# Optimization experiments

Measured on AMD Instinct MI355X. Metric: run time of the kernel, lower is better.

## Reference

```python
import jax, jax.numpy as jnp
import numpy as np

B, T, E, H, L, V, CTX = 16, 1024, 512, 8, 6, 32, 1024
HD = E // H


def setup_inputs() -> dict:
    key = jax.random.key(0)
    ks = jax.random.split(key, 20)
    s = 0.02
    inp = {
        "tokens": jax.random.randint(ks[0], (B, T), 0, V),
        "emb": jax.random.normal(ks[1], (V, E), jnp.float32) * s,
        "pos_emb": jax.random.normal(ks[2], (CTX, E), jnp.float32) * s,
        "Wq": jax.random.normal(ks[3], (L, H, E, HD), jnp.float32) * s,
        "Wk": jax.random.normal(ks[4], (L, H, E, HD), jnp.float32) * s,
        "Wv": jax.random.normal(ks[5], (L, H, E, HD), jnp.float32) * s,
        "Wo": jax.random.normal(ks[6], (L, E, E), jnp.float32) * s,
        "bo": jnp.zeros((L, E), jnp.float32),
        "ln1_g": jnp.ones((L, E), jnp.float32),
        "ln1_b": jnp.zeros((L, E), jnp.float32),
        "ln2_g": jnp.ones((L, E), jnp.float32),
        "ln2_b": jnp.zeros((L, E), jnp.float32),
        "W1": jax.random.normal(ks[7], (L, E, E), jnp.float32) * s,
        "b1": jnp.zeros((L, E), jnp.float32),
        "W2": jax.random.normal(ks[8], (L, E, E), jnp.float32) * s,
        "b2": jnp.zeros((L, E), jnp.float32),
        "lnf_g": jnp.ones((E,), jnp.float32),
        "lnf_b": jnp.zeros((E,), jnp.float32),
        "Wf": jax.random.normal(ks[9], (E, V), jnp.float32) * s,
        "bf": jnp.zeros((V,), jnp.float32),
    }
    return inp


def _layernorm(x, g, b, eps=1e-5):
    mu = x.mean(-1, keepdims=True)
    var = ((x - mu) ** 2).mean(-1, keepdims=True)
    return (x - mu) * jax.lax.rsqrt(var + eps) * g + b


def reference(tokens, emb, pos_emb, Wq, Wk, Wv, Wo, bo, ln1_g, ln1_b,
              ln2_g, ln2_b, W1, b1, W2, b2, lnf_g, lnf_b, Wf, bf):
    Bt, Tt = tokens.shape
    x = emb[tokens] + pos_emb[:Tt]  # [B,T,E]
    causal = jnp.tril(jnp.ones((Tt, Tt), bool))

    def block(x, p):
        wq, wk, wv, wo, bo_, g1, b1_, g2, b2_, w1, bb1, w2, bb2 = p
        h = _layernorm(x, g1, b1_)
        q = jnp.einsum('bte,hed->bhtd', h, wq)
        k = jnp.einsum('bte,hed->bhtd', h, wk)
        v = jnp.einsum('bte,hed->bhtd', h, wv)
        # NOTE: source applies NO 1/sqrt(d) scaling
        s = jnp.einsum('bhtd,bhsd->bhts', q, k)
        s = jnp.where(causal, s, -jnp.inf)
        a = jax.nn.softmax(s, axis=-1)
        o = jnp.einsum('bhts,bhsd->bhtd', a, v)
        o = o.transpose(0, 2, 1, 3).reshape(Bt, Tt, E)  # concat heads
        x = x + jnp.einsum('bte,ef->btf', o, wo) + bo_
        h2 = _layernorm(x, g2, b2_)
        f = jax.nn.relu(jnp.einsum('bte,ef->btf', h2, w1) + bb1)
        f = jnp.einsum('bte,ef->btf', f, w2) + bb2
        return x + f, None

    x, _ = jax.lax.scan(block, x, (Wq, Wk, Wv, Wo, bo, ln1_g, ln1_b,
                                   ln2_g, ln2_b, W1, b1, W2, b2))
    x = _layernorm(x, lnf_g, lnf_b)
    logits = jnp.einsum('bte,ev->btv', x, Wf) + bf
    return logits
```

## Files before the change

kernel.cpp:

```cpp
#include <hip/hip_runtime.h>
#include <hip/hip_bf16.h>

namespace {

constexpr int B = 16, T = 1024, E = 512, H = 8, L = 6, V = 32, HD = 64;
constexpr int BT = B * T;
constexpr long S = (long)BT * E;
constexpr int QS = 1536;

typedef __attribute__((ext_vector_type(8))) short bf16x8;
typedef __attribute__((ext_vector_type(4))) float f32x4;

__device__ inline float b2f(ushort u) {
  union { unsigned u; float f; } v; v.u = (unsigned)u << 16; return v.f;
}
__device__ inline ushort f2b(float f) {
  union { float f; unsigned u; } v; v.f = f;
  unsigned r = v.u + 0x7FFFu + ((v.u >> 16) & 1u);
  return (ushort)(r >> 16);
}
__device__ inline void gl_lds16(const ushort* g, ushort* lds) {
  __builtin_amdgcn_global_load_lds(
      (const __attribute__((address_space(1))) void*)g,
      (__attribute__((address_space(3))) void*)lds, 16, 0, 0);
}

__global__ void embed_kernel(const int* __restrict__ tokens,
                             const float* __restrict__ emb,
                             const float* __restrict__ pos,
                             float* __restrict__ x) {
  int idx = blockIdx.x * blockDim.x + threadIdx.x;
  constexpr int TOT = BT * (E / 4);
  if (idx >= TOT) return;
  int row = idx >> 7, c4 = idx & 127;
  int t = row & (T - 1);
  int tok = tokens[row];
  float4 a = reinterpret_cast<const float4*>(emb + (long)tok * E)[c4];
  float4 p = reinterpret_cast<const float4*>(pos + (long)t * E)[c4];
  float4 r;
  r.x = a.x + p.x; r.y = a.y + p.y; r.z = a.z + p.z; r.w = a.w + p.w;
  reinterpret_cast<float4*>(x + (long)row * E)[c4] = r;
}

__global__ __launch_bounds__(256)
void wconv_kernel(const float* __restrict__ in, ushort* __restrict__ out,
                  int K, int Nn, int ppl, long layer_stride, long off) {
  const int z = blockIdx.z;
  const long pin = (long)z * K * Nn;
  const long pout = (long)(z / ppl) * layer_stride + off +
                    (long)(z % ppl) * Nn * K;
  __shared__ float t[32][33];
  const int k0 = blockIdx.x * 32, n0 = blockIdx.y * 32;
  const int tid = threadIdx.x, r = tid >> 5, c = tid & 31;
  #pragma unroll
  for (int i = 0; i < 4; i++)
    t[r + i * 8][c] = in[pin + (long)(k0 + r + i * 8) * Nn + n0 + c];
  __syncthreads();
  #pragma unroll
  for (int i = 0; i < 4; i++)
    out[pout + (long)(n0 + r + i * 8) * K + k0 + c] = f2b(t[c][r + i * 8]);
}

__global__ __launch_bounds__(128)
void ln_kernel(const float* __restrict__ x, const float* __restrict__ g,
               const float* __restrict__ b, ushort* __restrict__ out) {
  int row = blockIdx.x, tid = threadIdx.x;
  float4 v = reinterpret_cast<const float4*>(x + (long)row * E)[tid];
  float s = v.x + v.y + v.z + v.w;
  #pragma unroll
  for (int off = 32; off > 0; off >>= 1) s += __shfl_down(s, off, 64);
  __shared__ float r1[2], r2[2];
  int lane = tid & 63, wid = tid >> 6;
  if (lane == 0) r1[wid] = s;
  __syncthreads();
  float mean = (r1[0] + r1[1]) * (1.0f / E);
  float4 d;
  d.x = v.x - mean; d.y = v.y - mean; d.z = v.z - mean; d.w = v.w - mean;
  float s2 = d.x * d.x + d.y * d.y + d.z * d.z + d.w * d.w;
  #pragma unroll
  for (int off = 32; off > 0; off >>= 1) s2 += __shfl_down(s2, off, 64);
  if (lane == 0) r2[wid] = s2;
  __syncthreads();
  float rstd = rsqrtf((r2[0] + r2[1]) * (1.0f / E) + 1e-5f);
  float4 gg = reinterpret_cast<const float4*>(g)[tid];
  float4 bb = reinterpret_cast<const float4*>(b)[tid];
  ushort4 o;
  o.x = f2b(d.x * rstd * gg.x + bb.x);
  o.y = f2b(d.y * rstd * gg.y + bb.y);
  o.z = f2b(d.z * rstd * gg.z + bb.z);
  o.w = f2b(d.w * rstd * gg.w + bb.w);
  reinterpret_cast<ushort4*>(out + (long)row * E)[tid] = o;
}

template <int MODE>
__global__ __launch_bounds__(256, 3)
void bgemm_kernel(const ushort* __restrict__ A, const ushort* __restrict__ Bt,
                  const float* __restrict__ bias, const float* __restrict__ res,
                  void* __restrict__ Cout, int Nl) {
  constexpr int K = 512;
  __shared__ ushort As[128][32];
  __shared__ ushort Bs[128][32];
  const int tid = threadIdx.x, lane = tid & 63, wid = tid >> 6;
  const int bm = blockIdx.x * 128, bn = blockIdx.y * 128;
  const int wm = (wid >> 1) * 64, wn = (wid & 1) * 64;
  const int lo = lane & 15, hi = lane >> 4;
  const int arow = lane >> 2, acol = (lane & 3) * 8;
  f32x4 acc[4][4] = {};
  for (int k0 = 0; k0 < K; k0 += 32) {
    #pragma unroll
    for (int i = 0; i < 2; i++) {
      int seg = wid * 2 + i;
      gl_lds16(A + (long)(bm + seg * 16 + arow) * K + k0 + acol,
               &As[seg * 16][0]);
      gl_lds16(Bt + (long)(bn + seg * 16 + arow) * K + k0 + acol,
               &Bs[seg * 16][0]);
    }
    __syncthreads();
    bf16x8 af[4], bfr[4];
    #pragma unroll
    for (int mi = 0; mi < 4; mi++)
      af[mi] = *(const bf16x8*)&As[wm + mi * 16 + lo][hi * 8];
    #pragma unroll
    for (int ni = 0; ni < 4; ni++)
      bfr[ni] = *(const bf16x8*)&Bs[wn + ni * 16 + lo][hi * 8];
    #pragma unroll
    for (int mi = 0; mi < 4; mi++)
      #pragma unroll
      for (int ni = 0; ni < 4; ni++)
        acc[mi][ni] = __builtin_amdgcn_mfma_f32_16x16x32_bf16(
            af[mi], bfr[ni], acc[mi][ni], 0, 0, 0);
    __syncthreads();
  }
  #pragma unroll
  for (int mi = 0; mi < 4; mi++) {
    #pragma unroll
    for (int ni = 0; ni < 4; ni++) {
      const int gn = bn + wn + ni * 16 + lo;
      const float bv = (MODE >= 1) ? bias[gn] : 0.f;
      #pragma unroll
      for (int r = 0; r < 4; r++) {
        const long gm = bm + wm + mi * 16 + hi * 4 + r;
        float vv = acc[mi][ni][r];
        if (MODE == 0) {
          ((ushort*)Cout)[gm * Nl + gn] = f2b(vv);
        } else if (MODE == 1) {
          ((float*)Cout)[gm * Nl + gn] = vv + bv + res[gm * Nl + gn];
        } else {
          ((ushort*)Cout)[gm * Nl + gn] = f2b(fmaxf(vv + bv, 0.f));
        }
      }
    }
  }
}

__global__ __launch_bounds__(256, 2)
void attn_kernel(const ushort* __restrict__ qkv, ushort* __restrict__ o) {
  const int b = blockIdx.z, h = blockIdx.y;
  const int qt = (gridDim.x - 1) - blockIdx.x;
  const int tid = threadIdx.x, wid = tid >> 6, lane = tid & 63;
  const int lo = lane & 15, hi = lane >> 4;
  const long bh = (long)b * T;
  const int qbase = qt * 128 + wid * 32;
  const int dch = qt * 2 + (wid >> 1);
  const int roff = 32 * (wid & 1);
  constexpr float SHIFT = 12.0f;
  __shared__ ushort Ks[64 * 64];
  __shared__ ushort Vs[64 * 64];
  __shared__ ushort Ps[4][32 * 64];
  char* KsB = (char*)Ks;
  char* VsB = (char*)Vs;
  char* PsB = (char*)Ps[wid];

  bf16x8 qf[2][2];
  #pragma unroll
  for (int mf = 0; mf < 2; mf++)
    #pragma unroll
    for (int kh = 0; kh < 2; kh++)
      qf[mf][kh] = *(const bf16x8*)(qkv + (bh + qbase + mf * 16 + lo) * QS +
                                    h * 64 + kh * 32 + hi * 8);
  f32x4 accO[2][4] = {};
  float lsum[2][4];
  #pragma unroll
  for (int a = 0; a < 2; a++)
    #pragma unroll
    for (int r = 0; r < 4; r++) lsum[a][r] = 0.f;

  const ushort* kb = qkv + bh * QS + 512 + h * 64;
  const ushort* vb = qkv + bh * QS + 1024 + h * 64;
  const int nch = qt * 2 + 2;

  for (int c = 0; c < nch; c++) {
    const long s0 = (long)c * 64;
    #pragma unroll
    for (int it = 0; it < 2; it++) {
      int idx = it * 256 + tid;
      int key = idx >> 3, c8 = idx & 7;
      uint4 kv = *(const uint4*)(kb + (s0 + key) * QS + c8 * 8);
      *(uint4*)(KsB + ((key * 128 + c8 * 16) ^ ((key & 7) << 4))) = kv;
    }
    {
      const int key0 = (tid & 31) * 2, dim0 = (tid >> 5) * 8;
      uint4 v0 = *(const uint4*)(vb + (s0 + key0) * QS + dim0);
      uint4 v1 = *(const uint4*)(vb + (s0 + key0 + 1) * QS + dim0);
      const ushort* p0 = (const ushort*)&v0;
      const ushort* p1 = (const ushort*)&v1;
      #pragma unroll
      for (int j = 0; j < 8; j++) {
        const int dim = dim0 + j;
        ushort2 w; w.x = p0[j]; w.y = p1[j];
        *(ushort2*)(VsB + ((dim * 128 + key0 * 2) ^ ((dim & 7) << 4))) = w;
      }
    }
    __syncthreads();
    if (c <= dch) {
      const bool diag = (c == dch);
      bf16x8 kf[4][2];
      #pragma unroll
      for (int nf = 0; nf < 4; nf++)
        #pragma unroll
        for (int kh = 0; kh < 2; kh++) {
          const int key = nf * 16 + lo;
          kf[nf][kh] = *(const bf16x8*)(
              KsB + ((key * 128 + kh * 64 + hi * 16) ^ ((key & 7) << 4)));
        }
      #pragma unroll
      for (int mf = 0; mf < 2; mf++) {
        f32x4 s[4];
        #pragma unroll
        for (int nf = 0; nf < 4; nf++) {
          f32x4 z = {0.f, 0.f, 0.f, 0.f};
          z = __builtin_amdgcn_mfma_f32_16x16x32_bf16(qf[mf][0], kf[nf][0],
                                                      z, 0, 0, 0);
          z = __builtin_amdgcn_mfma_f32_16x16x32_bf16(qf[mf][1], kf[nf][1],
                                                      z, 0, 0, 0);
          s[nf] = z;
        }
        if (diag) {
          #pragma unroll
          for (int nf = 0; nf < 4; nf++)
            #pragma unroll
            for (int r = 0; r < 4; r++)
              if (nf * 16 + lo > roff + mf * 16 + hi * 4 + r)
                s[nf][r] = -1e30f;
        }
        #pragma unroll
        for (int r = 0; r < 4; r++) {
          float p0 = __expf(s[0][r] - SHIFT), p1 = __expf(s[1][r] - SHIFT);
          float p2 = __expf(s[2][r] - SHIFT), p3 = __expf(s[3][r] - SHIFT);
          lsum[mf][r] += (p0 + p1) + (p2 + p3);
          const int ql = mf * 16 + hi * 4 + r;
          const int swz = (ql & 7) << 4;
          *(ushort*)(PsB + ((ql * 128 + (lo) * 2) ^ swz))      = f2b(p0);
          *(ushort*)(PsB + ((ql * 128 + (16 + lo) * 2) ^ swz)) = f2b(p1);
          *(ushort*)(PsB + ((ql * 128 + (32 + lo) * 2) ^ swz)) = f2b(p2);
          *(ushort*)(PsB + ((ql * 128 + (48 + lo) * 2) ^ swz)) = f2b(p3);
        }
      }
      asm volatile("s_waitcnt lgkmcnt(0)" ::: "memory");
      #pragma unroll
      for (int ks = 0; ks < 2; ks++) {
        bf16x8 pa[2];
        #pragma unroll
        for (int mf = 0; mf < 2; mf++) {
          const int ql = mf * 16 + lo;
          pa[mf] = *(const bf16x8*)(
              PsB + ((ql * 128 + ks * 64 + hi * 16) ^ ((ql & 7) << 4)));
        }
        #pragma unroll
        for (int nd = 0; nd < 4; nd++) {
          const int dim = nd * 16 + lo;
          bf16x8 vf = *(const bf16x8*)(
              VsB + ((dim * 128 + ks * 64 + hi * 16) ^ ((dim & 7) << 4)));
          #pragma unroll
          for (int mf = 0; mf < 2; mf++)
            accO[mf][nd] = __builtin_amdgcn_mfma_f32_16x16x32_bf16(
                pa[mf], vf, accO[mf][nd], 0, 0, 0);
        }
      }
    }
    __syncthreads();
  }
  #pragma unroll
  for (int mf = 0; mf < 2; mf++)
    #pragma unroll
    for (int r = 0; r < 4; r++) {
      float l = lsum[mf][r];
      #pragma unroll
      for (int msk = 1; msk < 16; msk <<= 1) l += __shfl_xor(l, msk, 64);
      lsum[mf][r] = 1.0f / l;
    }
  #pragma unroll
  for (int mf = 0; mf < 2; mf++)
    #pragma unroll
    for (int nd = 0; nd < 4; nd++)
      #pragma unroll
      for (int r = 0; r < 4; r++) {
        const int ql = mf * 16 + hi * 4 + r, dim = nd * 16 + lo;
        *(ushort*)(PsB + ql * 128 + dim * 2) =
            f2b(accO[mf][nd][r] * lsum[mf][r]);
      }
  asm volatile("s_waitcnt lgkmcnt(0)" ::: "memory");
  #pragma unroll
  for (int it = 0; it < 4; it++) {
    const int idx = it * 64 + lane;
    const int row = idx >> 3, c8 = idx & 7;
    uint4 val = *(const uint4*)(PsB + row * 128 + c8 * 16);
    *(uint4*)(o + (bh + qbase + row) * E + h * 64 + c8 * 8) = val;
  }
}

__global__ __launch_bounds__(256)
void logits_kernel(const ushort* __restrict__ xf, const ushort* __restrict__ WfT,
                   const float* __restrict__ bf, float* __restrict__ out) {
  __shared__ float xs[8][E];
  const int row0 = blockIdx.x * 8, tid = threadIdx.x;
  #pragma unroll
  for (int i = 0; i < 4; i++) {
    int idx = i * 256 + tid;
    int r = idx >> 7, c4 = idx & 127;
    ushort4 u = ((const ushort4*)(xf + (long)(row0 + r) * E))[c4];
    float4 f;
    f.x = b2f(u.x); f.y = b2f(u.y); f.z = b2f(u.z); f.w = b2f(u.w);
    *(float4*)&xs[r][c4 * 4] = f;
  }
  __syncthreads();
  const int r = tid >> 5, c = tid & 31;
  float acc = 0.f;
  for (int e8 = 0; e8 < 64; e8++) {
    uint4 w = *(const uint4*)(WfT + (long)c * E + e8 * 8);
    const ushort* ws = (const ushort*)&w;
    #pragma unroll
    for (int j = 0; j < 8; j++) acc += xs[r][e8 * 8 + j] * b2f(ws[j]);
  }
  out[(long)(row0 + r) * V + c] = acc + bf[c];
}

}

extern "C" void kernel_launch(void* const* d_in, const int* in_sizes, int n_in,
                              void* d_out, int out_size, void* d_ws,
                              size_t ws_size, hipStream_t stream) {
  const int*   tokens = (const int*)d_in[0];
  const float* emb    = (const float*)d_in[1];
  const float* pos    = (const float*)d_in[2];
  const float* Wq     = (const float*)d_in[3];
  const float* Wk     = (const float*)d_in[4];
  const float* Wv     = (const float*)d_in[5];
  const float* Wo     = (const float*)d_in[6];
  const float* bo     = (const float*)d_in[7];
  const float* ln1g   = (const float*)d_in[8];
  const float* ln1b   = (const float*)d_in[9];
  const float* ln2g   = (const float*)d_in[10];
  const float* ln2b   = (const float*)d_in[11];
  const float* W1     = (const float*)d_in[12];
  const float* b1     = (const float*)d_in[13];
  const float* W2     = (const float*)d_in[14];
  const float* b2     = (const float*)d_in[15];
  const float* lnfg   = (const float*)d_in[16];
  const float* lnfb   = (const float*)d_in[17];
  const float* Wf     = (const float*)d_in[18];
  const float* bf     = (const float*)d_in[19];
  float* out = (float*)d_out;

  char* p = (char*)d_ws;
  float*  x    = (float*)p;          p += S * 4;
  ushort* hb   = (ushort*)p;         p += S * 2;
  ushort* qkvb = (ushort*)p;         p += (long)BT * QS * 2;
  const long WSZ = (long)L * E * E;
  ushort* wqkvT = (ushort*)p;        p += (long)L * QS * E * 2;
  ushort* woT  = (ushort*)p;         p += WSZ * 2;
  ushort* w1T  = (ushort*)p;         p += WSZ * 2;
  ushort* w2T  = (ushort*)p;         p += WSZ * 2;
  ushort* wfT  = (ushort*)p;         p += (long)E * V * 2;

  const long QLS = (long)QS * E;

  wconv_kernel<<<dim3(16, 2, L * H), 256, 0, stream>>>(Wq, wqkvT, E, HD, H,
                                                       QLS, 0);
  wconv_kernel<<<dim3(16, 2, L * H), 256, 0, stream>>>(Wk, wqkvT, E, HD, H,
                                                       QLS, (long)512 * E);
  wconv_kernel<<<dim3(16, 2, L * H), 256, 0, stream>>>(Wv, wqkvT, E, HD, H,
                                                       QLS, (long)1024 * E);
  wconv_kernel<<<dim3(16, 16, L), 256, 0, stream>>>(Wo, woT, E, E, 1,
                                                    (long)E * E, 0);
  wconv_kernel<<<dim3(16, 16, L), 256, 0, stream>>>(W1, w1T, E, E, 1,
                                                    (long)E * E, 0);
  wconv_kernel<<<dim3(16, 16, L), 256, 0, stream>>>(W2, w2T, E, E, 1,
                                                    (long)E * E, 0);
  wconv_kernel<<<dim3(16, 1, 1), 256, 0, stream>>>(Wf, wfT, E, V, 1,
                                                   (long)E * V, 0);

  embed_kernel<<<(BT * (E / 4) + 255) / 256, 256, 0, stream>>>(tokens, emb,
                                                               pos, x);

  const dim3 gq(BT / 128, QS / 128);
  const dim3 gg(BT / 128, E / 128);
  const dim3 ga(T / 128, H, B);

  for (int l = 0; l < L; l++) {
    const long wo = (long)l * E * E;
    ln_kernel<<<BT, 128, 0, stream>>>(x, ln1g + l * E, ln1b + l * E, hb);
    bgemm_kernel<0><<<gq, 256, 0, stream>>>(hb, wqkvT + l * QLS, nullptr,
                                            nullptr, qkvb, QS);
    attn_kernel<<<ga, 256, 0, stream>>>(qkvb, hb);
    bgemm_kernel<1><<<gg, 256, 0, stream>>>(hb, woT + wo, bo + l * E, x, x,
                                            E);
    ln_kernel<<<BT, 128, 0, stream>>>(x, ln2g + l * E, ln2b + l * E, hb);
    bgemm_kernel<2><<<gg, 256, 0, stream>>>(hb, w1T + wo, b1 + l * E, nullptr,
                                            qkvb, E);
    bgemm_kernel<1><<<gg, 256, 0, stream>>>((ushort*)qkvb, w2T + wo,
                                            b2 + l * E, x, x, E);
  }

  ln_kernel<<<BT, 128, 0, stream>>>(x, lnfg, lnfb, hb);
  logits_kernel<<<BT / 8, 256, 0, stream>>>(hb, wfT, bf, out);
}
```

Before: 1.348 ms.

## Double GEMM K-tile to 64 and use 128-key attention chunks with diagonal trimming

The GEMM now stages a 64-wide K slice per iteration, halving the number of barrier-separated loop trips and issuing twice as many MFMAs between syncs. The attention kernel processes 128-key chunks instead of 64, so there are half as many K/V load and barrier rounds. On the diagonal chunk each wave limits its QK and PV loops to the keys it actually needs instead of idling. This costs more LDS per block (larger K, V and P tiles), which may lower occupancy, and the attention inner loops become runtime-bounded rather than fully unrolled.

After: 1.451 ms. 1.08x slower.

```diff
diff --git a/kernel.cpp b/kernel.cpp
--- a/kernel.cpp
+++ b/kernel.cpp
@@ -98,37 +98,43 @@
                   const float* __restrict__ bias, const float* __restrict__ res,
                   void* __restrict__ Cout, int Nl) {
   constexpr int K = 512;
-  __shared__ ushort As[128][32];
-  __shared__ ushort Bs[128][32];
+  __shared__ ushort As[128][64];
+  __shared__ ushort Bs[128][64];
   const int tid = threadIdx.x, lane = tid & 63, wid = tid >> 6;
   const int bm = blockIdx.x * 128, bn = blockIdx.y * 128;
   const int wm = (wid >> 1) * 64, wn = (wid & 1) * 64;
   const int lo = lane & 15, hi = lane >> 4;
-  const int arow = lane >> 2, acol = (lane & 3) * 8;
+  const int arow = lane >> 3, acol = (lane & 7) * 8;
   f32x4 acc[4][4] = {};
-  for (int k0 = 0; k0 < K; k0 += 32) {
-    #pragma unroll
-    for (int i = 0; i < 2; i++) {
-      int seg = wid * 2 + i;
-      gl_lds16(A + (long)(bm + seg * 16 + arow) * K + k0 + acol,
-               &As[seg * 16][0]);
-      gl_lds16(Bt + (long)(bn + seg * 16 + arow) * K + k0 + acol,
-               &Bs[seg * 16][0]);
+  for (int k0 = 0; k0 < K; k0 += 64) {
+    #pragma unroll
+    for (int i = 0; i < 4; i++) {
+      int seg = wid * 4 + i;
+      gl_lds16(A + (long)(bm + seg * 8 + arow) * K + k0 + acol,
+               &As[seg * 8][0]);
+      gl_lds16(Bt + (long)(bn + seg * 8 + arow) * K + k0 + acol,
+               &Bs[seg * 8][0]);
     }
     __syncthreads();
-    bf16x8 af[4], bfr[4];
+    bf16x8 af[4][2], bfr[4][2];
     #pragma unroll
     for (int mi = 0; mi < 4; mi++)
-      af[mi] = *(const bf16x8*)&As[wm + mi * 16 + lo][hi * 8];
+      #pragma unroll
+      for (int kh = 0; kh < 2; kh++)
+        af[mi][kh] = *(const bf16x8*)&As[wm + mi * 16 + lo][kh * 32 + hi * 8];
     #pragma unroll
     for (int ni = 0; ni < 4; ni++)
-      bfr[ni] = *(const bf16x8*)&Bs[wn + ni * 16 + lo][hi * 8];
-    #pragma unroll
-    for (int mi = 0; mi < 4; mi++)
-      #pragma unroll
-      for (int ni = 0; ni < 4; ni++)
-        acc[mi][ni] = __builtin_amdgcn_mfma_f32_16x16x32_bf16(
-            af[mi], bfr[ni], acc[mi][ni], 0, 0, 0);
+      #pragma unroll
+      for (int kh = 0; kh < 2; kh++)
+        bfr[ni][kh] = *(const bf16x8*)&Bs[wn + ni * 16 + lo][kh * 32 + hi * 8];
+    #pragma unroll
+    for (int kh = 0; kh < 2; kh++)
+      #pragma unroll
+      for (int mi = 0; mi < 4; mi++)
+        #pragma unroll
+        for (int ni = 0; ni < 4; ni++)
+          acc[mi][ni] = __builtin_amdgcn_mfma_f32_16x16x32_bf16(
+              af[mi][kh], bfr[ni][kh], acc[mi][ni], 0, 0, 0);
     __syncthreads();
   }
   #pragma unroll
@@ -161,12 +167,11 @@
   const int lo = lane & 15, hi = lane >> 4;
   const long bh = (long)b * T;
   const int qbase = qt * 128 + wid * 32;
-  const int dch = qt * 2 + (wid >> 1);
-  const int roff = 32 * (wid & 1);
+  const int roff = wid * 32;
   constexpr float SHIFT = 12.0f;
-  __shared__ ushort Ks[64 * 64];
-  __shared__ ushort Vs[64 * 64];
-  __shared__ ushort Ps[4][32 * 64];
+  __shared__ ushort Ks[128 * 64];
+  __shared__ ushort Vs[64 * 128];
+  __shared__ ushort Ps[4][32 * 128];
   char* KsB = (char*)Ks;
   char* VsB = (char*)Vs;
   char* PsB = (char*)Ps[wid];
@@ -187,90 +192,87 @@
 
   const ushort* kb = qkv + bh * QS + 512 + h * 64;
   const ushort* vb = qkv + bh * QS + 1024 + h * 64;
-  const int nch = qt * 2 + 2;
+  const int nch = qt + 1;
 
   for (int c = 0; c < nch; c++) {
-    const long s0 = (long)c * 64;
-    #pragma unroll
-    for (int it = 0; it < 2; it++) {
+    const long s0 = (long)c * 128;
+    #pragma unroll
+    for (int it = 0; it < 4; it++) {
       int idx = it * 256 + tid;
       int key = idx >> 3, c8 = idx & 7;
       uint4 kv = *(const uint4*)(kb + (s0 + key) * QS + c8 * 8);
       *(uint4*)(KsB + ((key * 128 + c8 * 16) ^ ((key & 7) << 4))) = kv;
     }
     {
-      const int key0 = (tid & 31) * 2, dim0 = (tid >> 5) * 8;
-      uint4 v0 = *(const uint4*)(vb + (s0 + key0) * QS + dim0);
-      uint4 v1 = *(const uint4*)(vb + (s0 + key0 + 1) * QS + dim0);
-      const ushort* p0 = (const ushort*)&v0;
-      const ushort* p1 = (const ushort*)&v1;
+      const int key0 = (tid & 63) * 2, dim0 = (tid >> 6) * 16;
+      uint4 va0 = *(const uint4*)(vb + (s0 + key0) * QS + dim0);
+      uint4 va1 = *(const uint4*)(vb + (s0 + key0) * QS + dim0 + 8);
+      uint4 vb0 = *(const uint4*)(vb + (s0 + key0 + 1) * QS + dim0);
+      uint4 vb1 = *(const uint4*)(vb + (s0 + key0 + 1) * QS + dim0 + 8);
+      const ushort* pa_ = (const ushort*)&va0;
+      const ushort* pa2 = (const ushort*)&va1;
+      const ushort* pb_ = (const ushort*)&vb0;
+      const ushort* pb2 = (const ushort*)&vb1;
       #pragma unroll
       for (int j = 0; j < 8; j++) {
         const int dim = dim0 + j;
-        ushort2 w; w.x = p0[j]; w.y = p1[j];
-        *(ushort2*)(VsB + ((dim * 128 + key0 * 2) ^ ((dim & 7) << 4))) = w;
+        ushort2 w; w.x = pa_[j]; w.y = pb_[j];
+        *(ushort2*)(VsB + ((dim * 256 + key0 * 2) ^ ((dim & 7) << 4))) = w;
+      }
+      #pragma unroll
+      for (int j = 0; j < 8; j++) {
+        const int dim = dim0 + 8 + j;
+        ushort2 w; w.x = pa2[j]; w.y = pb2[j];
+        *(ushort2*)(VsB + ((dim * 256 + key0 * 2) ^ ((dim & 7) << 4))) = w;
       }
     }
     __syncthreads();
-    if (c <= dch) {
-      const bool diag = (c == dch);
-      bf16x8 kf[4][2];
-      #pragma unroll
-      for (int nf = 0; nf < 4; nf++)
+    {
+      const bool diag = (c == qt);
+      const int nfLim = diag ? (roff / 16 + 2) : 8;
+      const int ksLim = diag ? (roff / 32 + 1) : 4;
+      for (int nf = 0; nf < nfLim; nf++) {
+        const int key = nf * 16 + lo;
+        const int kswz = (key & 7) << 4;
+        bf16x8 kf0 = *(const bf16x8*)(KsB + ((key * 128 + hi * 16) ^ kswz));
+        bf16x8 kf1 =
+            *(const bf16x8*)(KsB + ((key * 128 + 64 + hi * 16) ^ kswz));
         #pragma unroll
-        for (int kh = 0; kh < 2; kh++) {
-          const int key = nf * 16 + lo;
-          kf[nf][kh] = *(const bf16x8*)(
-              KsB + ((key * 128 + kh * 64 + hi * 16) ^ ((key & 7) << 4)));
-        }
-      #pragma unroll
-      for (int mf = 0; mf < 2; mf++) {
-        f32x4 s[4];
-        #pragma unroll
-        for (int nf = 0; nf < 4; nf++) {
+        for (int mf = 0; mf < 2; mf++) {
           f32x4 z = {0.f, 0.f, 0.f, 0.f};
-          z = __builtin_amdgcn_mfma_f32_16x16x32_bf16(qf[mf][0], kf[nf][0],
-                                                      z, 0, 0, 0);
-          z = __builtin_amdgcn_mfma_f32_16x16x32_bf16(qf[mf][1], kf[nf][1],
-                                                      z, 0, 0, 0);
-          s[nf] = z;
-        }
-        if (diag) {
-          #pragma unroll
-          for (int nf = 0; nf < 4; nf++)
+          z = __builtin_amdgcn_mfma_f32_16x16x32_bf16(qf[mf][0], kf0, z,
+                                                      0, 0, 0);
+          z = __builtin_amdgcn_mfma_f32_16x16x32_bf16(qf[mf][1], kf1, z,
+                                                      0, 0, 0);
+          if (diag) {
             #pragma unroll
             for (int r = 0; r < 4; r++)
-              if (nf * 16 + lo > roff + mf * 16 + hi * 4 + r)
-                s[nf][r] = -1e30f;
+              if (key > roff + mf * 16 + hi * 4 + r) z[r] = -1e30f;
+          }
+          #pragma unroll
+          for (int r = 0; r < 4; r++) {
+            float p = __expf(z[r] - SHIFT);
+            lsum[mf][r] += p;
+            const int ql = mf * 16 + hi * 4 + r;
+            *(ushort*)(PsB + ((ql * 256 + key * 2) ^ ((ql & 7) << 4))) =
+                f2b(p);
+          }
         }
-        #pragma unroll
-        for (int r = 0; r < 4; r++) {
-          float p0 = __expf(s[0][r] - SHIFT), p1 = __expf(s[1][r] - SHIFT);
-          float p2 = __expf(s[2][r] - SHIFT), p3 = __expf(s[3][r] - SHIFT);
-          lsum[mf][r] += (p0 + p1) + (p2 + p3);
-          const int ql = mf * 16 + hi * 4 + r;
-          const int swz = (ql & 7) << 4;
-          *(ushort*)(PsB + ((ql * 128 + (lo) * 2) ^ swz))      = f2b(p0);
-          *(ushort*)(PsB + ((ql * 128 + (16 + lo) * 2) ^ swz)) = f2b(p1);
-          *(ushort*)(PsB + ((ql * 128 + (32 + lo) * 2) ^ swz)) = f2b(p2);
-          *(ushort*)(PsB + ((ql * 128 + (48 + lo) * 2) ^ swz)) = f2b(p3);
-        }
       }
       asm volatile("s_waitcnt lgkmcnt(0)" ::: "memory");
-      #pragma unroll
-      for (int ks = 0; ks < 2; ks++) {
+      for (int ks = 0; ks < ksLim; ks++) {
         bf16x8 pa[2];
         #pragma unroll
         for (int mf = 0; mf < 2; mf++) {
           const int ql = mf * 16 + lo;
           pa[mf] = *(const bf16x8*)(
-              PsB + ((ql * 128 + ks * 64 + hi * 16) ^ ((ql & 7) << 4)));
+              PsB + ((ql * 256 + ks * 64 + hi * 16) ^ ((ql & 7) << 4)));
         }
         #pragma unroll
         for (int nd = 0; nd < 4; nd++) {
           const int dim = nd * 16 + lo;
           bf16x8 vf = *(const bf16x8*)(
-              VsB + ((dim * 128 + ks * 64 + hi * 16) ^ ((dim & 7) << 4)));
+              VsB + ((dim * 256 + ks * 64 + hi * 16) ^ ((dim & 7) << 4)));
           #pragma unroll
           for (int mf = 0; mf < 2; mf++)
             accO[mf][nd] = __builtin_amdgcn_mfma_f32_16x16x32_bf16(
```
